# Kernel tuning notes

Hardware: AMD Instinct MI355X
Metric: run time of the kernel (lower is better)

Reference implementation:

```python
import jax, jax.numpy as jnp
import numpy as np

B, N, C = 8, 4096, 256
HEADS = 8
DH = C // HEADS
SR = 4
EPS = 1e-5


def setup_inputs() -> dict:
    key = jax.random.key(0)
    ks = jax.random.split(key, 12)
    s = 0.02
    inp = {
        "x": jax.random.normal(ks[0], (B, N, C), dtype=jnp.float32),
        "H": 64,
        "W": 64,
        # nn.Linear weights stored torch-style [out, in]
        "q_w": jax.random.normal(ks[1], (C, C), dtype=jnp.float32) * s,
        "q_b": jax.random.normal(ks[2], (C,), dtype=jnp.float32) * s,
        "kv_w": jax.random.normal(ks[3], (2 * C, C), dtype=jnp.float32) * s,
        "kv_b": jax.random.normal(ks[4], (2 * C,), dtype=jnp.float32) * s,
        # Conv2d weight torch OIHW [C, C, SR, SR]
        "sr_w": jax.random.normal(ks[5], (C, C, SR, SR), dtype=jnp.float32) * s,
        "sr_b": jax.random.normal(ks[6], (C,), dtype=jnp.float32) * s,
        "ln_g": jnp.ones((C,), dtype=jnp.float32),
        "ln_b": jnp.zeros((C,), dtype=jnp.float32),
        "proj_w": jax.random.normal(ks[7], (C, C), dtype=jnp.float32) * s,
        "proj_b": jax.random.normal(ks[8], (C,), dtype=jnp.float32) * s,
    }
    return inp


def _layernorm(x, g, b):
    mu = jnp.mean(x, axis=-1, keepdims=True)
    var = jnp.mean(jnp.square(x - mu), axis=-1, keepdims=True)
    return (x - mu) * jax.lax.rsqrt(var + EPS) * g + b


def reference(x, H, W, q_w, q_b, kv_w, kv_b, sr_w, sr_b, ln_g, ln_b, proj_w, proj_b):
    b, n, c = x.shape
    scale = 1.0 / jnp.sqrt(jnp.float32(DH))

    # q projection -> [b, heads, n, dh]
    q = (x @ q_w.T + q_b).reshape(b, n, HEADS, DH).transpose(0, 2, 1, 3)

    # spatial reduction: conv stride=SR kernel=SR on the [b,H,W,c] image
    x_img = x.reshape(b, H, W, c)  # NHWC
    kern = jnp.transpose(sr_w, (2, 3, 1, 0))  # OIHW -> HWIO
    x_sr = jax.lax.conv_general_dilated(
        x_img, kern, window_strides=(SR, SR), padding="VALID",
        dimension_numbers=("NHWC", "HWIO", "NHWC")) + sr_b
    n_kv = (H // SR) * (W // SR)
    x_sr = x_sr.reshape(b, n_kv, c)
    x_sr = _layernorm(x_sr, ln_g, ln_b)

    # kv projection -> k, v: [b, heads, n_kv, dh]
    kv = (x_sr @ kv_w.T + kv_b).reshape(b, n_kv, 2, HEADS, DH)
    kv = kv.transpose(2, 0, 3, 1, 4)
    k, v = kv[0], kv[1]

    # attention (dropout rates are 0.0 / eval mode)
    attn = jnp.einsum("bhnd,bhmd->bhnm", q, k) * scale
    attn = jax.nn.softmax(attn, axis=-1)
    out = jnp.einsum("bhnm,bhmd->bhnd", attn, v)
    out = out.transpose(0, 2, 1, 3).reshape(b, n, c)
    return out @ proj_w.T + proj_b
```

## Files before the change

### kernel.cpp

```cpp
#include <hip/hip_runtime.h>

typedef unsigned short u16;
typedef float f32x4 __attribute__((ext_vector_type(4)));
typedef __bf16 bf16x4 __attribute__((ext_vector_type(4)));
typedef __bf16 bf16x8 __attribute__((ext_vector_type(8)));

#define B_ 8
#define N_ 4096
#define C_ 256
#define NKV 256
#define CEXP 0.25506604f

__device__ inline u16 f2bf(float f) {
    union { float f; unsigned u; } v; v.f = f;
    unsigned r = v.u + 0x7FFF + ((v.u >> 16) & 1);
    return (u16)(r >> 16);
}

__device__ inline void gload16(const void* g, void* l) {
    __builtin_amdgcn_global_load_lds(
        (const __attribute__((address_space(1))) void*)g,
        (__attribute__((address_space(3))) void*)l, 16, 0, 0);
}

__global__ __launch_bounds__(256) void prep_all(
    const float* __restrict__ x, u16* __restrict__ xb,
    const float* __restrict__ qw, const float* __restrict__ kvw,
    const float* __restrict__ pw, const float* __restrict__ srw,
    u16* __restrict__ wqb, u16* __restrict__ wkv, u16* __restrict__ wp, u16* __restrict__ wsr)
{
    size_t base = ((size_t)blockIdx.x * 256 + threadIdx.x) * 4;
    float4 v = *(const float4*)(x + base);
    ushort4 o;
    o.x = f2bf(v.x); o.y = f2bf(v.y); o.z = f2bf(v.z); o.w = f2bf(v.w);
    *(ushort4*)(xb + base) = o;

    int t = blockIdx.x * 256 + threadIdx.x;
    int stride = gridDim.x * 256;
    for (int i = t; i < 65536; i += stride) { wqb[i] = f2bf(qw[i]); wp[i] = f2bf(pw[i]); }
    for (int i = t; i < 131072; i += stride) wkv[i] = f2bf(kvw[i]);
    for (int i = t; i < 1048576; i += stride) {
        int oo = i >> 12, kk = i & 4095;
        int ci = kk & 255, khkw = kk >> 8;
        wsr[i] = f2bf(srw[(size_t)(oo * 256 + ci) * 16 + khkw]);
    }
}

template<int OUTMODE, bool SCALEK, bool IM2COL>
__global__ __launch_bounds__(256, 2) void gemm128(
    const u16* __restrict__ A, const u16* __restrict__ Bt,
    const float* __restrict__ bias, void* __restrict__ outp,
    int M, int Nn, int K, int kchunk)
{
    __shared__ __align__(16) u16 As[128 * 32];
    __shared__ __align__(16) u16 Bs[128 * 32];
    const int tid = threadIdx.x;
    const int bm = blockIdx.x, bn = blockIdx.y, bz = blockIdx.z;
    const int k0 = bz * kchunk;
    const int wid = tid >> 6, lane = tid & 63;
    const int wr = wid >> 1, wc = wid & 1;
    const int lrow = lane & 15, lkg = lane >> 4;

    f32x4 acc[4][4] = {};

    const int c1 = tid, c2 = tid + 256;
    const int r1 = c1 >> 2, cl1 = (c1 & 3) * 8;
    const int r2 = c2 >> 2, cl2 = (c2 & 3) * 8;
    const u16 *aS1, *aS2;
    if constexpr (IM2COL) {
        const int g1 = bm * 128 + r1, g2 = bm * 128 + r2;
        const int b1 = g1 >> 8, p1 = g1 & 255;
        const int b2 = g2 >> 8, p2 = g2 & 255;
        aS1 = A + ((size_t)(b1 * 4096 + (p1 >> 4) * 256 + (p1 & 15) * 4) * 256 + cl1);
        aS2 = A + ((size_t)(b2 * 4096 + (p2 >> 4) * 256 + (p2 & 15) * 4) * 256 + cl2);
    } else {
        aS1 = A + (size_t)(bm * 128 + r1) * K + k0 + cl1;
        aS2 = A + (size_t)(bm * 128 + r2) * K + k0 + cl2;
    }
    const u16* bS1 = Bt + (size_t)(bn * 128 + r1) * K + k0 + cl1;
    const u16* bS2 = Bt + (size_t)(bn * 128 + r2) * K + k0 + cl2;
    u16* aD1 = As + c1 * 8;  u16* aD2 = As + c2 * 8;
    u16* bD1 = Bs + c1 * 8;  u16* bD2 = Bs + c2 * 8;

    for (int kk = 0; kk < kchunk; kk += 32) {
        int aoff;
        if constexpr (IM2COL) {
            const int K0 = k0 + kk;
            const int khkw = K0 >> 8;
            aoff = ((khkw >> 2) * 64 + (khkw & 3)) * 256 + (K0 & 255);
        } else {
            aoff = kk;
        }
        gload16(aS1 + aoff, aD1);
        gload16(aS2 + aoff, aD2);
        gload16(bS1 + kk, bD1);
        gload16(bS2 + kk, bD2);
        __syncthreads();
        bf16x8 af[4], bff[4];
#pragma unroll
        for (int i = 0; i < 4; ++i) {
            af[i]  = *(const bf16x8*)(As + (wr * 64 + i * 16 + lrow) * 32 + lkg * 8);
            bff[i] = *(const bf16x8*)(Bs + (wc * 64 + i * 16 + lrow) * 32 + lkg * 8);
        }
#pragma unroll
        for (int i = 0; i < 4; ++i)
#pragma unroll
            for (int j = 0; j < 4; ++j)
                acc[i][j] = __builtin_amdgcn_mfma_f32_16x16x32_bf16(af[i], bff[j], acc[i][j], 0, 0, 0);
        __syncthreads();
    }

    const int row0 = bm * 128 + wr * 64;
    const int col0 = bn * 128 + wc * 64;
    if constexpr (OUTMODE == 2) {
        float* o = (float*)outp + (size_t)bz * M * Nn;
#pragma unroll
        for (int i = 0; i < 4; ++i)
#pragma unroll
            for (int j = 0; j < 4; ++j)
#pragma unroll
                for (int reg = 0; reg < 4; ++reg)
                    o[(size_t)(row0 + i * 16 + lkg * 4 + reg) * Nn + col0 + j * 16 + lrow] = acc[i][j][reg];
    } else {
#pragma unroll
        for (int j = 0; j < 4; ++j) {
            const int col = col0 + j * 16 + lrow;
            float bv = bias[col];
            float sc = 1.0f;
            if constexpr (SCALEK) { if (col < 256) sc = CEXP; }
#pragma unroll
            for (int i = 0; i < 4; ++i)
#pragma unroll
                for (int reg = 0; reg < 4; ++reg) {
                    const size_t idx = (size_t)(row0 + i * 16 + lkg * 4 + reg) * Nn + col;
                    const float val = (acc[i][j][reg] + bv) * sc;
                    if constexpr (OUTMODE == 1) ((u16*)outp)[idx] = f2bf(val);
                    else                        ((float*)outp)[idx] = val;
                }
        }
    }
}

__global__ __launch_bounds__(256) void ln_kernel(
    const float* __restrict__ part, const float* __restrict__ srb,
    const float* __restrict__ g, const float* __restrict__ bb, u16* __restrict__ out)
{
    const int row = blockIdx.x, c = threadIdx.x;
    const size_t idx = (size_t)row * 256 + c;
    float v = srb[c];
#pragma unroll
    for (int z = 0; z < 8; ++z) v += part[idx + (size_t)z * 524288];
    float s = v;
#pragma unroll
    for (int m = 1; m < 64; m <<= 1) s += __shfl_xor(s, m);
    __shared__ float red[4];
    if ((c & 63) == 0) red[c >> 6] = s;
    __syncthreads();
    float tot = red[0] + red[1] + red[2] + red[3];
    float mu = tot * (1.0f / 256.0f);
    float d = v - mu;
    float s2 = d * d;
#pragma unroll
    for (int m = 1; m < 64; m <<= 1) s2 += __shfl_xor(s2, m);
    __syncthreads();
    if ((c & 63) == 0) red[c >> 6] = s2;
    __syncthreads();
    float var = (red[0] + red[1] + red[2] + red[3]) * (1.0f / 256.0f);
    out[idx] = f2bf(d * rsqrtf(var + 1e-5f) * g[c] + bb[c]);
}

__global__ __launch_bounds__(256, 2) void attn_kernel(
    const u16* __restrict__ qbuf, const u16* __restrict__ kvbuf, u16* __restrict__ obuf)
{
    __shared__ __align__(16) u16 Ks[256 * 40];
    __shared__ __align__(16) u16 Vt[32 * 264];
    const int qt = blockIdx.x, h = blockIdx.y, b = blockIdx.z;
    const int tid = threadIdx.x;
    const int wid = tid >> 6, lane = tid & 63;
    const int lrow = lane & 15, lkg = lane >> 4;

    {
        const u16* ks = kvbuf + (size_t)(b * 256 + tid) * 512 + h * 32;
        u16* kd = Ks + tid * 40;
#pragma unroll
        for (int c = 0; c < 4; ++c)
            *(int4*)(kd + c * 8) = *(const int4*)(ks + c * 8);
    }
    {
        const u16* vs = kvbuf + (size_t)(b * 256 + tid) * 512 + 256 + h * 32;
#pragma unroll
        for (int j = 0; j < 8; ++j) {
            ushort4 vv = *(const ushort4*)(vs + j * 4);
            Vt[(j * 4 + 0) * 264 + tid] = vv.x;
            Vt[(j * 4 + 1) * 264 + tid] = vv.y;
            Vt[(j * 4 + 2) * 264 + tid] = vv.z;
            Vt[(j * 4 + 3) * 264 + tid] = vv.w;
        }
    }

    const int qcol = h * 32 + lkg * 8;
    bf16x8 qf = *(const bf16x8*)(qbuf +
        (size_t)(b * 4096 + qt * 64 + wid * 16 + lrow) * 256 + qcol);

    bf16x8 onesf = {};
    if (lrow == 0) {
#pragma unroll
        for (int e = 0; e < 8; ++e) onesf[e] = (__bf16)1.0f;
    }

    __syncthreads();

    f32x4 acc[16];
#pragma unroll
    for (int nf = 0; nf < 16; ++nf) acc[nf] = (f32x4){0.f, 0.f, 0.f, 0.f};
#pragma unroll
    for (int nf = 0; nf < 16; ++nf) {
        bf16x8 kfr = *(const bf16x8*)(Ks + (nf * 16 + lrow) * 40 + lkg * 8);
        acc[nf] = __builtin_amdgcn_mfma_f32_16x16x32_bf16(kfr, qf, acc[nf], 0, 0, 0);
    }

    bf16x8 pa8[8];
#pragma unroll
    for (int nf2 = 0; nf2 < 8; ++nf2) {
        bf16x8 pv;
#pragma unroll
        for (int half = 0; half < 2; ++half) {
#pragma unroll
            for (int r = 0; r < 4; ++r)
                pv[half * 4 + r] = (__bf16)exp2f(acc[2 * nf2 + half][r]);
        }
        pa8[nf2] = pv;
    }

    f32x4 o0 = (f32x4){0.f, 0.f, 0.f, 0.f};
    f32x4 o1 = (f32x4){0.f, 0.f, 0.f, 0.f};
    f32x4 o2 = (f32x4){0.f, 0.f, 0.f, 0.f};
#pragma unroll
    for (int nf2 = 0; nf2 < 8; ++nf2) {
        bf16x4 lo0 = *(const bf16x4*)(Vt + lrow * 264 + nf2 * 32 + lkg * 4);
        bf16x4 hi0 = *(const bf16x4*)(Vt + lrow * 264 + nf2 * 32 + 16 + lkg * 4);
        bf16x4 lo1 = *(const bf16x4*)(Vt + (16 + lrow) * 264 + nf2 * 32 + lkg * 4);
        bf16x4 hi1 = *(const bf16x4*)(Vt + (16 + lrow) * 264 + nf2 * 32 + 16 + lkg * 4);
        bf16x8 v0 = __builtin_shufflevector(lo0, hi0, 0, 1, 2, 3, 4, 5, 6, 7);
        bf16x8 v1 = __builtin_shufflevector(lo1, hi1, 0, 1, 2, 3, 4, 5, 6, 7);
        o0 = __builtin_amdgcn_mfma_f32_16x16x32_bf16(pa8[nf2], v0, o0, 0, 0, 0);
        o1 = __builtin_amdgcn_mfma_f32_16x16x32_bf16(pa8[nf2], v1, o1, 0, 0, 0);
        o2 = __builtin_amdgcn_mfma_f32_16x16x32_bf16(pa8[nf2], onesf, o2, 0, 0, 0);
    }

    float invq[4];
#pragma unroll
    for (int r = 0; r < 4; ++r)
        invq[r] = __shfl(__builtin_amdgcn_rcpf(o2[r]), lane & 48);

    const size_t obase = (size_t)(b * 4096 + qt * 64 + wid * 16);
#pragma unroll
    for (int r = 0; r < 4; ++r) {
        u16* op = obuf + (obase + lkg * 4 + r) * 256 + h * 32 + lrow;
        op[0]  = f2bf(o0[r] * invq[r]);
        op[16] = f2bf(o1[r] * invq[r]);
    }
}

extern "C" void kernel_launch(void* const* d_in, const int* in_sizes, int n_in,
                              void* d_out, int out_size, void* d_ws, size_t ws_size,
                              hipStream_t stream)
{
    (void)in_sizes; (void)n_in; (void)out_size; (void)ws_size;
    const float* x   = (const float*)d_in[0];
    const float* qw  = (const float*)d_in[3];
    const float* qb  = (const float*)d_in[4];
    const float* kvw = (const float*)d_in[5];
    const float* kvb = (const float*)d_in[6];
    const float* srw = (const float*)d_in[7];
    const float* srb = (const float*)d_in[8];
    const float* lng = (const float*)d_in[9];
    const float* lnb = (const float*)d_in[10];
    const float* pw  = (const float*)d_in[11];
    const float* pb  = (const float*)d_in[12];

    char* ws = (char*)d_ws;
    u16*   xb      = (u16*)(ws + 0);
    u16*   att     = (u16*)(ws + 16777216);
    float* part    = (float*)(ws + 33554432);
    u16*   wsr     = (u16*)(ws + 50331648);
    u16*   wqb     = (u16*)(ws + 52428800);
    u16*   wkvb    = (u16*)(ws + 52559872);
    u16*   wpb     = (u16*)(ws + 52822016);
    u16*   xsr     = (u16*)(ws + 52953088);
    u16*   kvo     = (u16*)(ws + 54001664);
    u16*   qbuf    = (u16*)d_out;

    prep_all<<<8192, 256, 0, stream>>>(x, xb, qw, kvw, pw, srw, wqb, wkvb, wpb, wsr);
    gemm128<2, false, true ><<<dim3(16, 2, 8), 256, 0, stream>>>(xb, wsr, nullptr, part, 2048, 256, 4096, 512);
    ln_kernel<<<2048, 256, 0, stream>>>(part, srb, lng, lnb, xsr);
    gemm128<1, true,  false><<<dim3(16, 4, 1), 256, 0, stream>>>(xsr, wkvb, kvb, kvo, 2048, 512, 256, 256);
    gemm128<1, false, false><<<dim3(256, 2, 1), 256, 0, stream>>>(xb, wqb, qb, qbuf, 32768, 256, 256, 256);
    attn_kernel<<<dim3(64, 8, 8), 256, 0, stream>>>(qbuf, kvo, att);
    gemm128<0, false, false><<<dim3(256, 2, 1), 256, 0, stream>>>(att, wpb, pb, d_out, 32768, 256, 256, 256);
}
```

Measured before the change: 100.8 us.

## Fuse conv split-K GEMM with Q projection into one launch; async K staging

The strided-conv split-K GEMM (now split 4 ways instead of 8) and the Q-projection GEMM run as one heterogeneous launch of 640 blocks, so the two independent GEMMs can overlap and one launch disappears. LayerNorm now reduces only 4 partial sums. The attention kernel stages K tiles with global_load_lds direct-to-LDS copies into an unpadded layout instead of register round-trips into a padded one. The unpadded K layout may cause LDS bank conflicts, and the larger conv K-chunk gives each conv block more serial work.

```diff
diff --git a/kernel.cpp b/kernel.cpp
--- a/kernel.cpp
+++ b/kernel.cpp
@@ -47,15 +47,13 @@
 }
 
 template<int OUTMODE, bool SCALEK, bool IM2COL>
-__global__ __launch_bounds__(256, 2) void gemm128(
+__device__ __forceinline__ void gemm_body(
+    u16* As, u16* Bs,
     const u16* __restrict__ A, const u16* __restrict__ Bt,
     const float* __restrict__ bias, void* __restrict__ outp,
-    int M, int Nn, int K, int kchunk)
-{
-    __shared__ __align__(16) u16 As[128 * 32];
-    __shared__ __align__(16) u16 Bs[128 * 32];
+    int M, int Nn, int K, int kchunk, int bm, int bn, int bz)
+{
     const int tid = threadIdx.x;
-    const int bm = blockIdx.x, bn = blockIdx.y, bz = blockIdx.z;
     const int k0 = bz * kchunk;
     const int wid = tid >> 6, lane = tid & 63;
     const int wr = wid >> 1, wc = wid & 1;
@@ -141,6 +139,36 @@
     }
 }
 
+template<int OUTMODE, bool SCALEK, bool IM2COL>
+__global__ __launch_bounds__(256, 2) void gemm128(
+    const u16* __restrict__ A, const u16* __restrict__ Bt,
+    const float* __restrict__ bias, void* __restrict__ outp,
+    int M, int Nn, int K, int kchunk)
+{
+    __shared__ __align__(16) u16 As[128 * 32];
+    __shared__ __align__(16) u16 Bs[128 * 32];
+    gemm_body<OUTMODE, SCALEK, IM2COL>(As, Bs, A, Bt, bias, outp, M, Nn, K, kchunk,
+                                       blockIdx.x, blockIdx.y, blockIdx.z);
+}
+
+__global__ __launch_bounds__(256, 2) void fused_convq(
+    const u16* __restrict__ xb, const u16* __restrict__ wsr, float* __restrict__ part,
+    const u16* __restrict__ wqb, const float* __restrict__ qb, u16* __restrict__ qbuf)
+{
+    __shared__ __align__(16) u16 As[128 * 32];
+    __shared__ __align__(16) u16 Bs[128 * 32];
+    const int id = blockIdx.x;
+    if (id < 128) {
+        const int z = id & 3, t = id >> 2;
+        gemm_body<2, false, true>(As, Bs, xb, wsr, nullptr, part,
+                                  2048, 256, 4096, 1024, t >> 1, t & 1, z);
+    } else {
+        const int qid = id - 128;
+        gemm_body<1, false, false>(As, Bs, xb, wqb, qb, qbuf,
+                                   32768, 256, 256, 256, qid >> 1, qid & 1, 0);
+    }
+}
+
 __global__ __launch_bounds__(256) void ln_kernel(
     const float* __restrict__ part, const float* __restrict__ srb,
     const float* __restrict__ g, const float* __restrict__ bb, u16* __restrict__ out)
@@ -149,7 +177,7 @@
     const size_t idx = (size_t)row * 256 + c;
     float v = srb[c];
 #pragma unroll
-    for (int z = 0; z < 8; ++z) v += part[idx + (size_t)z * 524288];
+    for (int z = 0; z < 4; ++z) v += part[idx + (size_t)z * 524288];
     float s = v;
 #pragma unroll
     for (int m = 1; m < 64; m <<= 1) s += __shfl_xor(s, m);
@@ -172,7 +200,7 @@
 __global__ __launch_bounds__(256, 2) void attn_kernel(
     const u16* __restrict__ qbuf, const u16* __restrict__ kvbuf, u16* __restrict__ obuf)
 {
-    __shared__ __align__(16) u16 Ks[256 * 40];
+    __shared__ __align__(16) u16 Ks[256 * 32];
     __shared__ __align__(16) u16 Vt[32 * 264];
     const int qt = blockIdx.x, h = blockIdx.y, b = blockIdx.z;
     const int tid = threadIdx.x;
@@ -180,11 +208,13 @@
     const int lrow = lane & 15, lkg = lane >> 4;
 
     {
-        const u16* ks = kvbuf + (size_t)(b * 256 + tid) * 512 + h * 32;
-        u16* kd = Ks + tid * 40;
-#pragma unroll
-        for (int c = 0; c < 4; ++c)
-            *(int4*)(kd + c * 8) = *(const int4*)(ks + c * 8);
+        const int rsub = lane >> 2, piece = lane & 3;
+#pragma unroll
+        for (int i = 0; i < 4; ++i) {
+            const int c = wid * 4 + i;
+            const u16* src = kvbuf + (size_t)(b * 256 + c * 16 + rsub) * 512 + h * 32 + piece * 8;
+            gload16(src, Ks + c * 512 + lane * 8);
+        }
     }
     {
         const u16* vs = kvbuf + (size_t)(b * 256 + tid) * 512 + 256 + h * 32;
@@ -215,7 +245,7 @@
     for (int nf = 0; nf < 16; ++nf) acc[nf] = (f32x4){0.f, 0.f, 0.f, 0.f};
 #pragma unroll
     for (int nf = 0; nf < 16; ++nf) {
-        bf16x8 kfr = *(const bf16x8*)(Ks + (nf * 16 + lrow) * 40 + lkg * 8);
+        bf16x8 kfr = *(const bf16x8*)(Ks + (nf * 16 + lrow) * 32 + lkg * 8);
         acc[nf] = __builtin_amdgcn_mfma_f32_16x16x32_bf16(kfr, qf, acc[nf], 0, 0, 0);
     }
 
@@ -292,10 +322,9 @@
     u16*   qbuf    = (u16*)d_out;
 
     prep_all<<<8192, 256, 0, stream>>>(x, xb, qw, kvw, pw, srw, wqb, wkvb, wpb, wsr);
-    gemm128<2, false, true ><<<dim3(16, 2, 8), 256, 0, stream>>>(xb, wsr, nullptr, part, 2048, 256, 4096, 512);
+    fused_convq<<<640, 256, 0, stream>>>(xb, wsr, part, wqb, qb, qbuf);
     ln_kernel<<<2048, 256, 0, stream>>>(part, srb, lng, lnb, xsr);
     gemm128<1, true,  false><<<dim3(16, 4, 1), 256, 0, stream>>>(xsr, wkvb, kvb, kvo, 2048, 512, 256, 256);
-    gemm128<1, false, false><<<dim3(256, 2, 1), 256, 0, stream>>>(xb, wqb, qb, qbuf, 32768, 256, 256, 256);
     attn_kernel<<<dim3(64, 8, 8), 256, 0, stream>>>(qbuf, kvo, att);
     gemm128<0, false, false><<<dim3(256, 2, 1), 256, 0, stream>>>(att, wpb, pb, d_out, 32768, 256, 256, 256);
 }
```

After: 95.22 us. 1.06x faster.
